# Kernel tuning notes

Hardware: AMD Instinct MI355X
Metric: run time of the kernel (lower is better)

Reference implementation:

```python
import jax, jax.numpy as jnp
import numpy as np

D_MODEL, D_STATE, D_CONV, EXPAND = 1024, 16, 4, 2
D_INNER = EXPAND * D_MODEL
B, L = 2, 2048
DT = 0.1  # module hard-codes dt = 0.1 (dt_proj is unused)


def setup_inputs() -> dict:
    key = jax.random.key(0)
    ks = jax.random.split(key, 7)
    s = 0.02
    x = jax.random.normal(ks[0], (B, L, D_MODEL), dtype=jnp.float32)
    in_proj_w = jax.random.normal(ks[1], (2 * D_INNER, D_MODEL), dtype=jnp.float32) * s
    conv_w = jax.random.normal(ks[2], (D_INNER, 1, D_CONV), dtype=jnp.float32) * s
    conv_b = jnp.zeros((D_INNER,), dtype=jnp.float32)
    x_proj_w = jax.random.normal(ks[3], (2 * D_STATE, D_INNER), dtype=jnp.float32) * s
    A_log = jnp.log(jnp.tile(jnp.arange(1, D_STATE + 1, dtype=jnp.float32), (D_INNER, 1)))
    D_param = jnp.ones((D_INNER,), dtype=jnp.float32)
    out_proj_w = jax.random.normal(ks[4], (D_MODEL, D_INNER), dtype=jnp.float32) * s
    return {"x": x, "in_proj_w": in_proj_w, "conv_w": conv_w, "conv_b": conv_b,
            "x_proj_w": x_proj_w, "A_log": A_log, "D_param": D_param,
            "out_proj_w": out_proj_w}


def _silu(v):
    return v * jax.nn.sigmoid(v)


def reference(x, in_proj_w, conv_w, conv_b, x_proj_w, A_log, D_param, out_proj_w):
    # in_proj: (B,L,d_model) -> (B,L,2*d_inner)
    xz = jnp.einsum('bld,ed->ble', x, in_proj_w)
    xs, z = jnp.split(xz, 2, axis=-1)
    # depthwise causal conv1d (torch pads both sides d_conv-1 then slices [:L] == left-pad only)
    xc = jax.lax.conv_general_dilated(
        xs.transpose(0, 2, 1), conv_w, window_strides=(1,),
        padding=[(D_CONV - 1, 0)], dimension_numbers=('NCH', 'OIH', 'NCH'),
        feature_group_count=D_INNER) + conv_b[None, :, None]
    xs = _silu(xc.transpose(0, 2, 1))  # (B, L, d_inner)
    # x_proj -> B_proj, C_proj  (B,L,d_state) each
    x_dbl = jnp.einsum('bld,ed->ble', xs, x_proj_w)
    B_proj, C_proj = jnp.split(x_dbl, 2, axis=-1)
    # SSM scan; dt is constant 0.1 so dA = exp(dt*A) is time-invariant
    A = -jnp.exp(A_log)                 # (d_inner, d_state)
    dA = jnp.exp(DT * A)                # (d_inner, d_state)

    def step(h, inp):
        x_t, B_t, C_t = inp             # (B,D), (B,N), (B,N)
        h = dA[None] * h + DT * B_t[:, None, :] * x_t[:, :, None]
        y_t = jnp.einsum('bdn,bn->bd', h, C_t)
        return h, y_t

    h0 = jnp.zeros((B, D_INNER, D_STATE), dtype=xs.dtype)
    _, ys = jax.lax.scan(step, h0,
                         (xs.transpose(1, 0, 2), B_proj.transpose(1, 0, 2), C_proj.transpose(1, 0, 2)))
    y = ys.transpose(1, 0, 2) + xs * D_param[None, None, :]
    y = y * _silu(z)
    return jnp.einsum('bld,ed->ble', y, out_proj_w)
```

## Files before the change

kernel.cpp:

```cpp
#include <hip/hip_runtime.h>
#include <hip/hip_bf16.h>
#include <math.h>

#define D_MODEL 1024
#define D_STATE 16
#define D_CONV  4
#define D_INNER 2048
#define BATCH   2
#define SEQ     2048
#define M_TOTAL (BATCH*SEQ)
#define DT_VAL  0.1f

#define CHUNK 64
#define WARM  64
#define NCHUNK (SEQ / CHUNK)
#define TSTEP 8

typedef __attribute__((ext_vector_type(8))) __bf16 bf16x8;
typedef __attribute__((ext_vector_type(4))) __bf16 bf16x4;
typedef __attribute__((ext_vector_type(4))) float floatx4;

__device__ __forceinline__ void gld_lds16(const __bf16* g, __bf16* l) {
    __builtin_amdgcn_global_load_lds(
        (const __attribute__((address_space(1))) void*)g,
        (__attribute__((address_space(3))) void*)l, 16, 0, 0);
}

__global__ __launch_bounds__(512, 2) void inproj_8p(
    const __bf16* __restrict__ A, const __bf16* __restrict__ W,
    __bf16* __restrict__ O1, __bf16* __restrict__ O2)
{
    __shared__ __bf16 As[4][256][32];
    __shared__ __bf16 Bs[4][256][32];
    constexpr int LDA = 1024;
    constexpr int NT  = 1024 / 32;

    const int tid = threadIdx.x;
    const int bid = blockIdx.x;
    const int xcd = bid & 7;
    const int idx = bid >> 3;
    const int mt  = xcd * 2 + (idx >> 4);
    const int nt  = idx & 15;
    const int m0  = mt * 256;
    const int n0  = nt * 256;

    const int wave = tid >> 6;
    const int lane = tid & 63;
    const int wr   = (wave >> 2) * 128;
    const int wc   = (wave & 3) * 64;
    const int fm   = lane & 15;
    const int coff = (((lane >> 4) ^ ((fm >> 1) & 3)) << 3);

    const int srow = tid >> 2;
    const int sc   = tid & 3;
    const int sgc  = sc ^ ((srow >> 1) & 3);
    const __bf16* ga = A + (size_t)(m0 + srow) * LDA + sgc * 8;
    const __bf16* gb = W + (size_t)(n0 + srow) * LDA + sgc * 8;
    __bf16* la = &As[0][srow][sc * 8];
    __bf16* lb = &Bs[0][srow][sc * 8];
    const size_t rstep = (size_t)128 * LDA;

    const __bf16* fa0 = &As[0][wr + fm][0] + coff;
    const __bf16* fb0 = &Bs[0][wc + fm][0] + coff;

    floatx4 acc[8][4];
    #pragma unroll
    for (int a = 0; a < 8; ++a)
        #pragma unroll
        for (int b = 0; b < 4; ++b)
            acc[a][b] = (floatx4){0.f, 0.f, 0.f, 0.f};

#define STAGE_A(u) { const int _b = (u) & 3; const int _k = (u) * 32;          \
        gld_lds16(ga + _k,         la + _b * 8192);                            \
        gld_lds16(ga + _k + rstep, la + _b * 8192 + 4096); }
#define STAGE_B(u) { const int _b = (u) & 3; const int _k = (u) * 32;          \
        gld_lds16(gb + _k,         lb + _b * 8192);                            \
        gld_lds16(gb + _k + rstep, lb + _b * 8192 + 4096); }

    STAGE_A(0); STAGE_B(0);
    STAGE_A(1); STAGE_B(1);
    STAGE_A(2); STAGE_B(2);
    asm volatile("s_waitcnt vmcnt(8)" ::: "memory");
    __builtin_amdgcn_s_barrier();

    #pragma unroll 4
    for (int t = 0; t < NT; ++t) {
        const int cur = t & 3;
        const __bf16* fA = fa0 + cur * 8192;
        const __bf16* fB = fb0 + cur * 8192;
        bf16x8 bfr[4], afr[4];

        #pragma unroll
        for (int b = 0; b < 4; ++b) bfr[b] = *(const bf16x8*)(fB + b * 512);
        #pragma unroll
        for (int a = 0; a < 4; ++a) afr[a] = *(const bf16x8*)(fA + a * 512);
        if (t + 3 < NT) STAGE_A(t + 3);
        asm volatile("" ::: "memory");
        __builtin_amdgcn_s_barrier();
        __builtin_amdgcn_s_setprio(1);
        #pragma unroll
        for (int a = 0; a < 4; ++a)
            #pragma unroll
            for (int b = 0; b < 4; ++b)
                acc[a][b] = __builtin_amdgcn_mfma_f32_16x16x32_bf16(
                    afr[a], bfr[b], acc[a][b], 0, 0, 0);
        __builtin_amdgcn_s_setprio(0);

        #pragma unroll
        for (int a = 0; a < 4; ++a) afr[a] = *(const bf16x8*)(fA + (4 + a) * 512);
        if (t + 3 < NT) STAGE_B(t + 3);
        asm volatile("" ::: "memory");
        __builtin_amdgcn_s_barrier();
        __builtin_amdgcn_s_setprio(1);
        #pragma unroll
        for (int a = 0; a < 4; ++a)
            #pragma unroll
            for (int b = 0; b < 4; ++b)
                acc[4 + a][b] = __builtin_amdgcn_mfma_f32_16x16x32_bf16(
                    afr[a], bfr[b], acc[4 + a][b], 0, 0, 0);
        __builtin_amdgcn_s_setprio(0);

        if (t < NT - 3) {
            asm volatile("s_waitcnt vmcnt(8)" ::: "memory");
        } else if (t == NT - 3) {
            asm volatile("s_waitcnt vmcnt(4)" ::: "memory");
        } else if (t == NT - 2) {
            asm volatile("s_waitcnt vmcnt(0)" ::: "memory");
        }
        if (t < NT - 1) __builtin_amdgcn_s_barrier();
    }
#undef STAGE_A
#undef STAGE_B

    const int crow = (lane >> 4) << 2;
    const int ccol = lane & 15;
    #pragma unroll
    for (int a = 0; a < 8; ++a) {
        #pragma unroll
        for (int b = 0; b < 4; ++b) {
            const int cm = m0 + wr + a * 16 + crow;
            const int cn = n0 + wc + b * 16 + ccol;
            #pragma unroll
            for (int r = 0; r < 4; ++r) {
                const float v = acc[a][b][r];
                if (n0 < 2048) {
                    O1[(size_t)(cm + r) * 2048 + cn] = (__bf16)v;
                } else {
                    const float s = v / (1.f + __expf(-v));
                    O2[(size_t)(cm + r) * 2048 + cn - 2048] = (__bf16)s;
                }
            }
        }
    }
}

template<int EPI, int LDA, int LDW, int KLEN, int NBX>
__global__ __launch_bounds__(256) void gemm_v5(
    const __bf16* __restrict__ A, const __bf16* __restrict__ W,
    float* __restrict__ Cf, float* __restrict__ Cf2, int ldc,
    __bf16* __restrict__ O1, __bf16* __restrict__ O2)
{
    __shared__ __bf16 As[2][128][32];
    __shared__ __bf16 Bs[2][128][32];

    const int tid  = threadIdx.x;
    const int bid  = blockIdx.x;
    const int xcd  = bid & 7;
    const int i    = bid >> 3;
    const int byl  = i & 3;
    const int rest = i >> 2;
    const int bx   = rest % NBX;
    const int ks   = rest / NBX;
    const int m0   = (xcd * 4 + byl) * 128;
    const int n0   = bx * 128;
    const int koff = ks * KLEN;

    const int wave = tid >> 6;
    const int lane = tid & 63;
    const int wr   = (wave >> 1) << 6;
    const int wc   = (wave & 1) << 6;
    const int fm   = lane & 15;
    const int fk   = (lane >> 4) << 3;
    const int grow = lane >> 2;
    const int gcol = (lane & 3) << 3;
    const int arow = wave * 16 + grow;

    floatx4 acc[4][4];
    #pragma unroll
    for (int a = 0; a < 4; ++a)
        #pragma unroll
        for (int b = 0; b < 4; ++b)
            acc[a][b] = (floatx4){0.f, 0.f, 0.f, 0.f};

    const __bf16* ap = A + (size_t)(m0 + arow) * LDA + koff + gcol;
    const __bf16* wp = W + (size_t)(n0 + arow) * LDW + koff + gcol;

    for (int k0 = 0; k0 < KLEN; k0 += 64) {
        __syncthreads();
        #pragma unroll
        for (int p = 0; p < 2; ++p) {
            gld_lds16(ap + k0 + p * 32,                    &As[p][arow][gcol]);
            gld_lds16(ap + k0 + p * 32 + (size_t)64 * LDA, &As[p][arow + 64][gcol]);
            gld_lds16(wp + k0 + p * 32,                    &Bs[p][arow][gcol]);
            gld_lds16(wp + k0 + p * 32 + (size_t)64 * LDW, &Bs[p][arow + 64][gcol]);
        }
        __syncthreads();

        #pragma unroll
        for (int p = 0; p < 2; ++p) {
            bf16x8 af[4], bfv[4];
            #pragma unroll
            for (int a = 0; a < 4; ++a)
                af[a] = *(bf16x8*)&As[p][wr + a * 16 + fm][fk];
            #pragma unroll
            for (int b = 0; b < 4; ++b)
                bfv[b] = *(bf16x8*)&Bs[p][wc + b * 16 + fm][fk];
            #pragma unroll
            for (int a = 0; a < 4; ++a)
                #pragma unroll
                for (int b = 0; b < 4; ++b)
                    acc[a][b] = __builtin_amdgcn_mfma_f32_16x16x32_bf16(
                        af[a], bfv[b], acc[a][b], 0, 0, 0);
        }
    }

    const int crow = (lane >> 4) << 2;
    const int ccol = lane & 15;
    #pragma unroll
    for (int a = 0; a < 4; ++a) {
        #pragma unroll
        for (int b = 0; b < 4; ++b) {
            const int cm = m0 + wr + a * 16 + crow;
            const int cn = n0 + wc + b * 16 + ccol;
            #pragma unroll
            for (int r = 0; r < 4; ++r) {
                const float v = acc[a][b][r];
                if (EPI == 1) {
                    if (n0 < 2048) {
                        O1[(size_t)(cm + r) * 2048 + cn] = (__bf16)v;
                    } else {
                        const float s = v / (1.f + __expf(-v));
                        O2[(size_t)(cm + r) * 2048 + cn - 2048] = (__bf16)s;
                    }
                } else {
                    float* dst = (ks < 2 ? Cf : Cf2) +
                                 (size_t)(ks & 1) * M_TOTAL * ldc;
                    dst[(size_t)(cm + r) * ldc + cn] = v;
                }
            }
        }
    }
}

__global__ __launch_bounds__(256) void reduce4(
    const float* __restrict__ p01, const float* __restrict__ p23,
    float* __restrict__ out)
{
    const size_t i = (size_t)(blockIdx.x * 256 + threadIdx.x) * 4;
    const float4 a = *(const float4*)(p01 + i);
    const float4 b = *(const float4*)(p01 + (size_t)M_TOTAL * D_MODEL + i);
    const float4 c = *(const float4*)(p23 + i);
    const float4 d = *(const float4*)(p23 + (size_t)M_TOTAL * D_MODEL + i);
    float4 o;
    o.x = (a.x + b.x) + (c.x + d.x);
    o.y = (a.y + b.y) + (c.y + d.y);
    o.z = (a.z + b.z) + (c.z + d.z);
    o.w = (a.w + b.w) + (c.w + d.w);
    *(float4*)(out + i) = o;
}

__global__ __launch_bounds__(256) void xproj_mfma(
    const __bf16* __restrict__ X, const __bf16* __restrict__ Wp,
    float* __restrict__ bc)
{
    __shared__ __bf16 Ash[128][32];
    __shared__ __bf16 Wsh[32][264];

    const int tid  = threadIdx.x;
    const int bid  = blockIdx.x;
    const int ks   = bid & 7;
    const int mb   = bid >> 3;
    const int m0   = mb * 128;
    const int koff = ks * 256;
    const int wave = tid >> 6;
    const int lane = tid & 63;
    const int fm   = lane & 15;
    const int fk   = (lane >> 4) << 3;
    const int grow = lane >> 2;
    const int gcol = (lane & 3) << 3;

    {
        const int r = tid >> 3;
        const int c = (tid & 7) << 5;
        #pragma unroll
        for (int q = 0; q < 4; ++q)
            *(bf16x8*)&Wsh[r][c + q * 8] =
                *(const bf16x8*)(Wp + (size_t)r * D_INNER + koff + c + q * 8);
    }

    floatx4 acc[2][2];
    #pragma unroll
    for (int a = 0; a < 2; ++a)
        #pragma unroll
        for (int b = 0; b < 2; ++b)
            acc[a][b] = (floatx4){0.f, 0.f, 0.f, 0.f};

    for (int kit = 0; kit < 8; ++kit) {
        const int kg = koff + kit * 32;
        __syncthreads();
        #pragma unroll
        for (int issue = 0; issue < 2; ++issue) {
            const int r = issue * 64 + wave * 16 + grow;
            gld_lds16(X + (size_t)(m0 + r) * D_INNER + kg + gcol, &Ash[r][gcol]);
        }
        __syncthreads();

        bf16x8 af[2], wf[2];
        af[0] = *(bf16x8*)&Ash[wave * 32 + fm][fk];
        af[1] = *(bf16x8*)&Ash[wave * 32 + 16 + fm][fk];
        wf[0] = *(bf16x8*)&Wsh[fm][kit * 32 + fk];
        wf[1] = *(bf16x8*)&Wsh[16 + fm][kit * 32 + fk];
        #pragma unroll
        for (int a = 0; a < 2; ++a)
            #pragma unroll
            for (int b = 0; b < 2; ++b)
                acc[a][b] = __builtin_amdgcn_mfma_f32_16x16x32_bf16(
                    af[a], wf[b], acc[a][b], 0, 0, 0);
    }

    const int crow = (lane >> 4) << 2;
    const int ccol = lane & 15;
    #pragma unroll
    for (int a = 0; a < 2; ++a)
        #pragma unroll
        for (int b = 0; b < 2; ++b)
            #pragma unroll
            for (int r = 0; r < 4; ++r)
                atomicAdd(bc + (size_t)(m0 + wave * 32 + a * 16 + crow + r) * 32
                             + b * 16 + ccol, acc[a][b][r]);
}

__global__ __launch_bounds__(256) void cast5(
    const float* __restrict__ x, const float* __restrict__ win,
    const float* __restrict__ wout, const float* __restrict__ xpw,
    __bf16* __restrict__ xbf, __bf16* __restrict__ winbf,
    __bf16* __restrict__ woutbf, __bf16* __restrict__ xpwbf,
    float* __restrict__ bcz)
{
    const size_t g = (size_t)(blockIdx.x * 256 + threadIdx.x);
    if (g >= 2637824) {
        const size_t off = (g - 2637824) * 4;
        *(float4*)(bcz + off) = (float4){0.f, 0.f, 0.f, 0.f};
        return;
    }
    const size_t j = g * 4;
    const float* src; __bf16* dst; size_t off;
    if (j < 4194304)       { src = x;    dst = xbf;    off = j; }
    else if (j < 8388608)  { src = win;  dst = winbf;  off = j - 4194304; }
    else if (j < 10485760) { src = wout; dst = woutbf; off = j - 8388608; }
    else                   { src = xpw;  dst = xpwbf;  off = j - 10485760; }
    const float4 v = *(const float4*)(src + off);
    bf16x4 o;
    o[0] = (__bf16)v.x; o[1] = (__bf16)v.y; o[2] = (__bf16)v.z; o[3] = (__bf16)v.w;
    *(bf16x4*)(dst + off) = o;
}

__global__ __launch_bounds__(256) void conv_silu4(
    const __bf16* __restrict__ xsp, const float* __restrict__ cw,
    const float* __restrict__ cb, __bf16* __restrict__ xsc)
{
    const int g    = blockIdx.x * 256 + threadIdx.x;
    const int d4   = g & (D_INNER / 4 - 1);
    const int mblk = g >> 9;
    const int m0   = mblk << 2;
    const int d    = d4 << 2;

    const float4 w0 = *(const float4*)(cw + (size_t)(d + 0) * 4);
    const float4 w1 = *(const float4*)(cw + (size_t)(d + 1) * 4);
    const float4 w2 = *(const float4*)(cw + (size_t)(d + 2) * 4);
    const float4 w3 = *(const float4*)(cw + (size_t)(d + 3) * 4);
    const float4 bv = *(const float4*)(cb + d);

    float4 rows[7];
    const int lbase = m0 & (SEQ - 1);
    #pragma unroll
    for (int j = 0; j < 7; ++j) {
        if (lbase + j >= 3) {
            const bf16x4 v = *(const bf16x4*)(xsp + (size_t)(m0 + j - 3) * D_INNER + d);
            rows[j].x = (float)v[0]; rows[j].y = (float)v[1];
            rows[j].z = (float)v[2]; rows[j].w = (float)v[3];
        } else {
            rows[j] = (float4){0.f, 0.f, 0.f, 0.f};
        }
    }

    #pragma unroll
    for (int o = 0; o < 4; ++o) {
        float a0 = bv.x, a1 = bv.y, a2 = bv.z, a3 = bv.w;
        #pragma unroll
        for (int j = 0; j < 4; ++j) {
            const float4 v = rows[o + j];
            const float wj0 = (j==0)?w0.x:(j==1)?w0.y:(j==2)?w0.z:w0.w;
            const float wj1 = (j==0)?w1.x:(j==1)?w1.y:(j==2)?w1.z:w1.w;
            const float wj2 = (j==0)?w2.x:(j==1)?w2.y:(j==2)?w2.z:w2.w;
            const float wj3 = (j==0)?w3.x:(j==1)?w3.y:(j==2)?w3.z:w3.w;
            a0 = fmaf(wj0, v.x, a0);
            a1 = fmaf(wj1, v.y, a1);
            a2 = fmaf(wj2, v.z, a2);
            a3 = fmaf(wj3, v.w, a3);
        }
        a0 = a0 / (1.f + __expf(-a0));
        a1 = a1 / (1.f + __expf(-a1));
        a2 = a2 / (1.f + __expf(-a2));
        a3 = a3 / (1.f + __expf(-a3));
        bf16x4 ob;
        ob[0] = (__bf16)a0; ob[1] = (__bf16)a1;
        ob[2] = (__bf16)a2; ob[3] = (__bf16)a3;
        *(bf16x4*)(xsc + (size_t)(m0 + o) * D_INNER + d) = ob;
    }
}

__global__ __launch_bounds__(256) void ssm_scan(
    const __bf16* __restrict__ xsc, const float* __restrict__ bc,
    const __bf16* __restrict__ szbf, __bf16* __restrict__ ybf,
    const float* __restrict__ alog, const float* __restrict__ dpar)
{
    __shared__ float Bsh[CHUNK + WARM][16];
    __shared__ float Csh[CHUNK + WARM][16];
    __shared__ float Xsh[2][TSTEP][256];
    __shared__ float Zsh[2][TSTEP][256];

    const int tid = threadIdx.x;
    const int blk = blockIdx.x;
    const int db  = blk & 7;
    const int ch  = (blk >> 3) & (NCHUNK - 1);
    const int b   = blk >> 8;
    const int d0  = db * 256;
    const int d   = d0 + tid;
    const int t0  = ch * CHUNK;
    const int tw  = (t0 >= WARM) ? (t0 - WARM) : 0;
    const int warm = t0 - tw;
    const int nt  = t0 + CHUNK - tw;
    const int ntiles = nt / TSTEP;

    const float* bcp = bc + ((size_t)b * SEQ + tw) * 32;
    for (int i = tid; i < nt * 8; i += 256) {
        const int row = i >> 3, q = i & 7;
        const float4 v = *(const float4*)(bcp + (size_t)row * 32 + q * 4);
        if (q < 4) *(float4*)&Bsh[row][q * 4] = v;
        else       *(float4*)&Csh[row][(q - 4) * 4] = v;
    }

    float dAv[16], h[16];
    #pragma unroll
    for (int q = 0; q < 4; ++q) {
        const float4 av = *(const float4*)(alog + (size_t)d * D_STATE + q * 4);
        dAv[q*4+0] = expf(-DT_VAL * expf(av.x));
        dAv[q*4+1] = expf(-DT_VAL * expf(av.y));
        dAv[q*4+2] = expf(-DT_VAL * expf(av.z));
        dAv[q*4+3] = expf(-DT_VAL * expf(av.w));
    }
    #pragma unroll
    for (int n = 0; n < 16; ++n) h[n] = 0.f;
    const float Dd = dpar[d];

    const __bf16* xbase = xsc  + ((size_t)b * SEQ + tw) * D_INNER + d0;
    const __bf16* zbase = szbf + ((size_t)b * SEQ + tw) * D_INNER + d0;
    __bf16*       ybase = ybf  + ((size_t)b * SEQ + tw) * D_INNER + d0;

    const int lrow = tid >> 6;
    const int lcol = (tid & 63) << 2;

    {
        const bf16x4 xa = *(const bf16x4*)(xbase + (size_t)lrow * D_INNER + lcol);
        const bf16x4 xb = *(const bf16x4*)(xbase + (size_t)(lrow + 4) * D_INNER + lcol);
        float4 fa, fb;
        fa.x=(float)xa[0]; fa.y=(float)xa[1]; fa.z=(float)xa[2]; fa.w=(float)xa[3];
        fb.x=(float)xb[0]; fb.y=(float)xb[1]; fb.z=(float)xb[2]; fb.w=(float)xb[3];
        *(float4*)&Xsh[0][lrow][lcol]     = fa;
        *(float4*)&Xsh[0][lrow + 4][lcol] = fb;
        if (warm == 0) {
            const bf16x4 za = *(const bf16x4*)(zbase + (size_t)lrow * D_INNER + lcol);
            const bf16x4 zb = *(const bf16x4*)(zbase + (size_t)(lrow + 4) * D_INNER + lcol);
            float4 ga, gb;
            ga.x=(float)za[0]; ga.y=(float)za[1]; ga.z=(float)za[2]; ga.w=(float)za[3];
            gb.x=(float)zb[0]; gb.y=(float)zb[1]; gb.z=(float)zb[2]; gb.w=(float)zb[3];
            *(float4*)&Zsh[0][lrow][lcol]     = ga;
            *(float4*)&Zsh[0][lrow + 4][lcol] = gb;
        }
    }
    __syncthreads();

    for (int tile = 0; tile < ntiles; ++tile) {
        const int buf = tile & 1;
        const int s   = tile * TSTEP;
        const int s2  = s + TSTEP;
        const bool more = (tile + 1 < ntiles);
        const bool znext = more && (s2 >= warm);

        bf16x4 rx0, rx1, rz0, rz1;
        if (more) {
            rx0 = *(const bf16x4*)(xbase + (size_t)(s2 + lrow) * D_INNER + lcol);
            rx1 = *(const bf16x4*)(xbase + (size_t)(s2 + lrow + 4) * D_INNER + lcol);
        }
        if (znext) {
            rz0 = *(const bf16x4*)(zbase + (size_t)(s2 + lrow) * D_INNER + lcol);
            rz1 = *(const bf16x4*)(zbase + (size_t)(s2 + lrow + 4) * D_INNER + lcol);
        }

        #pragma unroll
        for (int tt = 0; tt < TSTEP; ++tt) {
            const int t = s + tt;
            const float x   = Xsh[buf][tt][tid];
            const float dtx = DT_VAL * x;
            float y0 = 0.f, y1 = 0.f, y2 = 0.f, y3 = 0.f;
            #pragma unroll
            for (int n = 0; n < 4; ++n) {
                h[n]      = fmaf(dAv[n],      h[n],      dtx * Bsh[t][n]);
                h[n + 4]  = fmaf(dAv[n + 4],  h[n + 4],  dtx * Bsh[t][n + 4]);
                h[n + 8]  = fmaf(dAv[n + 8],  h[n + 8],  dtx * Bsh[t][n + 8]);
                h[n + 12] = fmaf(dAv[n + 12], h[n + 12], dtx * Bsh[t][n + 12]);
                y0 = fmaf(h[n],      Csh[t][n],      y0);
                y1 = fmaf(h[n + 4],  Csh[t][n + 4],  y1);
                y2 = fmaf(h[n + 8],  Csh[t][n + 8],  y2);
                y3 = fmaf(h[n + 12], Csh[t][n + 12], y3);
            }
            if (t >= warm) {
                const float sz = Zsh[buf][tt][tid];
                const float y  = fmaf(x, Dd, (y0 + y1) + (y2 + y3));
                ybase[(size_t)t * D_INNER + tid] = (__bf16)(y * sz);
            }
        }

        if (more) {
            float4 fa, fb;
            fa.x=(float)rx0[0]; fa.y=(float)rx0[1]; fa.z=(float)rx0[2]; fa.w=(float)rx0[3];
            fb.x=(float)rx1[0]; fb.y=(float)rx1[1]; fb.z=(float)rx1[2]; fb.w=(float)rx1[3];
            *(float4*)&Xsh[buf ^ 1][lrow][lcol]     = fa;
            *(float4*)&Xsh[buf ^ 1][lrow + 4][lcol] = fb;
        }
        if (znext) {
            float4 ga, gb;
            ga.x=(float)rz0[0]; ga.y=(float)rz0[1]; ga.z=(float)rz0[2]; ga.w=(float)rz0[3];
            gb.x=(float)rz1[0]; gb.y=(float)rz1[1]; gb.z=(float)rz1[2]; gb.w=(float)rz1[3];
            *(float4*)&Zsh[buf ^ 1][lrow][lcol]     = ga;
            *(float4*)&Zsh[buf ^ 1][lrow + 4][lcol] = gb;
        }
        __syncthreads();
    }
}

extern "C" void kernel_launch(void* const* d_in, const int* in_sizes, int n_in,
                              void* d_out, int out_size, void* d_ws, size_t ws_size,
                              hipStream_t stream)
{
    const float* x    = (const float*)d_in[0];
    const float* win  = (const float*)d_in[1];
    const float* cw   = (const float*)d_in[2];
    const float* cb   = (const float*)d_in[3];
    const float* xpw  = (const float*)d_in[4];
    const float* alog = (const float*)d_in[5];
    const float* dpar = (const float*)d_in[6];
    const float* wout = (const float*)d_in[7];
    float* out = (float*)d_out;

    char* w = (char*)d_ws;
    float*  pbuf   = (float*)w;
    __bf16* szbf   = (__bf16*)(w + 33554432);
    __bf16* xspbf  = (__bf16*)(w + 50331648);
    __bf16* xsc    = (__bf16*)(w + 67108864);
    float*  pbuf2  = (float*)(w + 50331648);
    float*  bcbuf  = (float*)(w + 83886080);
    __bf16* r1     = (__bf16*)(w + 84410368);
    __bf16* xbf    = r1;
    __bf16* winbf  = r1 + 4194304;
    __bf16* ybf    = r1;
    __bf16* woutbf = (__bf16*)(w + 101187584);
    __bf16* xpwbf  = (__bf16*)(w + 105381888);

    cast5<<<10432, 256, 0, stream>>>(x, win, wout, xpw,
                                     xbf, winbf, woutbf, xpwbf, bcbuf);
    inproj_8p<<<256, 512, 0, stream>>>(xbf, winbf, xspbf, szbf);
    conv_silu4<<<(M_TOTAL / 4 * (D_INNER / 4)) / 256, 256, 0, stream>>>(
        xspbf, cw, cb, xsc);
    xproj_mfma<<<256, 256, 0, stream>>>(xsc, xpwbf, bcbuf);
    ssm_scan<<<BATCH * NCHUNK * 8, 256, 0, stream>>>(
        xsc, bcbuf, szbf, ybf, alog, dpar);
    gemm_v5<2, 2048, 2048, 512, 8><<<1024, 256, 0, stream>>>(
        ybf, woutbf, pbuf, pbuf2, D_MODEL, nullptr, nullptr);
    reduce4<<<(M_TOTAL * D_MODEL / 4) / 256, 256, 0, stream>>>(pbuf, pbuf2, out);
}
```

Before: 235.4 us.

## Restructure in-proj GEMM into double-buffered 64-wide K tiles split in halves

Replaces the 4-stage ring of 32-wide K tiles in the input-projection GEMM with a 2-stage double buffer of 64-wide K tiles, each processed as two 32-wide halves. Each loop iteration prefetches the next full tile half by half while computing on the current one, which halves the iteration count but adds extra barriers per iteration. The effective prefetch depth drops from three tiles ahead to one, so global-load latency may be hidden less well, though LDS usage stays the same.

```diff
diff --git a/kernel.cpp b/kernel.cpp
--- a/kernel.cpp
+++ b/kernel.cpp
@@ -26,14 +26,14 @@
         (__attribute__((address_space(3))) void*)l, 16, 0, 0);
 }
 
-__global__ __launch_bounds__(512, 2) void inproj_8p(
+__global__ __launch_bounds__(512, 2) void inproj_kh(
     const __bf16* __restrict__ A, const __bf16* __restrict__ W,
     __bf16* __restrict__ O1, __bf16* __restrict__ O2)
 {
-    __shared__ __bf16 As[4][256][32];
-    __shared__ __bf16 Bs[4][256][32];
+    __shared__ __bf16 As[2][2][256][32];
+    __shared__ __bf16 Bs[2][2][256][32];
     constexpr int LDA = 1024;
-    constexpr int NT  = 1024 / 32;
+    constexpr int NT  = 16;
 
     const int tid = threadIdx.x;
     const int bid = blockIdx.x;
@@ -56,12 +56,12 @@
     const int sgc  = sc ^ ((srow >> 1) & 3);
     const __bf16* ga = A + (size_t)(m0 + srow) * LDA + sgc * 8;
     const __bf16* gb = W + (size_t)(n0 + srow) * LDA + sgc * 8;
-    __bf16* la = &As[0][srow][sc * 8];
-    __bf16* lb = &Bs[0][srow][sc * 8];
     const size_t rstep = (size_t)128 * LDA;
-
-    const __bf16* fa0 = &As[0][wr + fm][0] + coff;
-    const __bf16* fb0 = &Bs[0][wc + fm][0] + coff;
+    __bf16* la = &As[0][0][srow][sc * 8];
+    __bf16* lb = &Bs[0][0][srow][sc * 8];
+
+    const __bf16* fa_base = &As[0][0][wr + fm][0] + coff;
+    const __bf16* fb_base = &Bs[0][0][wc + fm][0] + coff;
 
     floatx4 acc[8][4];
     #pragma unroll
@@ -70,31 +70,34 @@
         for (int b = 0; b < 4; ++b)
             acc[a][b] = (floatx4){0.f, 0.f, 0.f, 0.f};
 
-#define STAGE_A(u) { const int _b = (u) & 3; const int _k = (u) * 32;          \
-        gld_lds16(ga + _k,         la + _b * 8192);                            \
-        gld_lds16(ga + _k + rstep, la + _b * 8192 + 4096); }
-#define STAGE_B(u) { const int _b = (u) & 3; const int _k = (u) * 32;          \
-        gld_lds16(gb + _k,         lb + _b * 8192);                            \
-        gld_lds16(gb + _k + rstep, lb + _b * 8192 + 4096); }
-
-    STAGE_A(0); STAGE_B(0);
-    STAGE_A(1); STAGE_B(1);
-    STAGE_A(2); STAGE_B(2);
-    asm volatile("s_waitcnt vmcnt(8)" ::: "memory");
+#define STAGE_A(u, kh) if ((u) < NT) {                                         \
+        const int _d = (((u) & 1) << 14) + ((kh) << 13);                       \
+        const size_t _g = (size_t)(u) * 64 + (kh) * 32;                        \
+        gld_lds16(ga + _g,         la + _d);                                   \
+        gld_lds16(ga + _g + rstep, la + _d + 4096); }
+#define STAGE_B(u, kh) if ((u) < NT) {                                         \
+        const int _d = (((u) & 1) << 14) + ((kh) << 13);                       \
+        const size_t _g = (size_t)(u) * 64 + (kh) * 32;                        \
+        gld_lds16(gb + _g,         lb + _d);                                   \
+        gld_lds16(gb + _g + rstep, lb + _d + 4096); }
+
+    STAGE_A(0, 0); STAGE_B(0, 0);
+    STAGE_A(0, 1); STAGE_B(0, 1);
+    asm volatile("s_waitcnt vmcnt(4)" ::: "memory");
     __builtin_amdgcn_s_barrier();
 
-    #pragma unroll 4
+    #pragma unroll 2
     for (int t = 0; t < NT; ++t) {
-        const int cur = t & 3;
-        const __bf16* fA = fa0 + cur * 8192;
-        const __bf16* fB = fb0 + cur * 8192;
-        bf16x8 bfr[4], afr[4];
+        const int s = t & 1;
+        const __bf16* fA = fa_base + (s << 14);
+        const __bf16* fB = fb_base + (s << 14);
+        bf16x8 afr[4], bfr[4];
 
         #pragma unroll
         for (int b = 0; b < 4; ++b) bfr[b] = *(const bf16x8*)(fB + b * 512);
         #pragma unroll
         for (int a = 0; a < 4; ++a) afr[a] = *(const bf16x8*)(fA + a * 512);
-        if (t + 3 < NT) STAGE_A(t + 3);
+        STAGE_A(t + 1, 0);
         asm volatile("" ::: "memory");
         __builtin_amdgcn_s_barrier();
         __builtin_amdgcn_s_setprio(1);
@@ -105,10 +108,11 @@
                 acc[a][b] = __builtin_amdgcn_mfma_f32_16x16x32_bf16(
                     afr[a], bfr[b], acc[a][b], 0, 0, 0);
         __builtin_amdgcn_s_setprio(0);
+        __builtin_amdgcn_s_barrier();
 
         #pragma unroll
         for (int a = 0; a < 4; ++a) afr[a] = *(const bf16x8*)(fA + (4 + a) * 512);
-        if (t + 3 < NT) STAGE_B(t + 3);
+        STAGE_B(t + 1, 0);
         asm volatile("" ::: "memory");
         __builtin_amdgcn_s_barrier();
         __builtin_amdgcn_s_setprio(1);
@@ -119,15 +123,44 @@
                 acc[4 + a][b] = __builtin_amdgcn_mfma_f32_16x16x32_bf16(
                     afr[a], bfr[b], acc[4 + a][b], 0, 0, 0);
         __builtin_amdgcn_s_setprio(0);
-
-        if (t < NT - 3) {
-            asm volatile("s_waitcnt vmcnt(8)" ::: "memory");
-        } else if (t == NT - 3) {
-            asm volatile("s_waitcnt vmcnt(4)" ::: "memory");
-        } else if (t == NT - 2) {
-            asm volatile("s_waitcnt vmcnt(0)" ::: "memory");
-        }
-        if (t < NT - 1) __builtin_amdgcn_s_barrier();
+        if (t < NT - 1) { asm volatile("s_waitcnt vmcnt(4)" ::: "memory"); }
+        else            { asm volatile("s_waitcnt vmcnt(0)" ::: "memory"); }
+        __builtin_amdgcn_s_barrier();
+
+        const __bf16* fA1 = fA + 8192;
+        const __bf16* fB1 = fB + 8192;
+        #pragma unroll
+        for (int b = 0; b < 4; ++b) bfr[b] = *(const bf16x8*)(fB1 + b * 512);
+        #pragma unroll
+        for (int a = 0; a < 4; ++a) afr[a] = *(const bf16x8*)(fA1 + a * 512);
+        STAGE_A(t + 1, 1);
+        asm volatile("" ::: "memory");
+        __builtin_amdgcn_s_barrier();
+        __builtin_amdgcn_s_setprio(1);
+        #pragma unroll
+        for (int a = 0; a < 4; ++a)
+            #pragma unroll
+            for (int b = 0; b < 4; ++b)
+                acc[a][b] = __builtin_amdgcn_mfma_f32_16x16x32_bf16(
+                    afr[a], bfr[b], acc[a][b], 0, 0, 0);
+        __builtin_amdgcn_s_setprio(0);
+        __builtin_amdgcn_s_barrier();
+
+        #pragma unroll
+        for (int a = 0; a < 4; ++a) afr[a] = *(const bf16x8*)(fA1 + (4 + a) * 512);
+        STAGE_B(t + 1, 1);
+        asm volatile("" ::: "memory");
+        __builtin_amdgcn_s_barrier();
+        __builtin_amdgcn_s_setprio(1);
+        #pragma unroll
+        for (int a = 0; a < 4; ++a)
+            #pragma unroll
+            for (int b = 0; b < 4; ++b)
+                acc[4 + a][b] = __builtin_amdgcn_mfma_f32_16x16x32_bf16(
+                    afr[a], bfr[b], acc[4 + a][b], 0, 0, 0);
+        __builtin_amdgcn_s_setprio(0);
+        if (t < NT - 1) { asm volatile("s_waitcnt vmcnt(4)" ::: "memory"); }
+        __builtin_amdgcn_s_barrier();
     }
 #undef STAGE_A
 #undef STAGE_B
@@ -580,7 +613,7 @@
 
     cast5<<<10432, 256, 0, stream>>>(x, win, wout, xpw,
                                      xbf, winbf, woutbf, xpwbf, bcbuf);
-    inproj_8p<<<256, 512, 0, stream>>>(xbf, winbf, xspbf, szbf);
+    inproj_kh<<<256, 512, 0, stream>>>(xbf, winbf, xspbf, szbf);
     conv_silu4<<<(M_TOTAL / 4 * (D_INNER / 4)) / 256, 256, 0, stream>>>(
         xspbf, cw, cb, xsc);
     xproj_mfma<<<256, 256, 0, stream>>>(xsc, xpwbf, bcbuf);
```

New measurement: 239.9 us. Within noise of the previous version (+1.9%).
